# Kernel tuning notes

Hardware: AMD Instinct MI355X
Metric: run time of the kernel (lower is better)

Reference implementation:

```python
import jax, jax.numpy as jnp
import numpy as np

D_MODEL = 1024
NUM_HEADS = 16
HEAD_DIM = D_MODEL // NUM_HEADS  # 64
SCALE = HEAD_DIM ** -0.5
BIAS_LEN = 128  # min(max_seq_len=512, 128)
ROPE_BASE = 10000.0
LN_EPS = 1e-5


def setup_inputs() -> dict:
    key = jax.random.key(0)
    ks = jax.random.split(key, 8)
    B, Lq, Lkv = 8, 512, 512
    return {
        "decoder_hidden": jax.random.normal(ks[0], (B, Lq, D_MODEL), jnp.float32),
        "encoder_output": jax.random.normal(ks[1], (B, Lkv, D_MODEL), jnp.float32),
        "Wqkv": jax.random.normal(ks[2], (3 * D_MODEL, D_MODEL), jnp.float32) * 0.02,
        "Wout": jax.random.normal(ks[3], (D_MODEL, D_MODEL), jnp.float32) * 0.02,
        "b_out": jnp.zeros((D_MODEL,), jnp.float32),
        "Wgate": jax.random.normal(ks[4], (D_MODEL, D_MODEL), jnp.float32) * 0.02,
        "b_gate": jnp.zeros((D_MODEL,), jnp.float32),
        "gamma": jnp.ones((D_MODEL,), jnp.float32),
        "beta": jnp.zeros((D_MODEL,), jnp.float32),
    }


def _layernorm(x, gamma, beta):
    mu = jnp.mean(x, axis=-1, keepdims=True)
    var = jnp.mean(jnp.square(x - mu), axis=-1, keepdims=True)
    return (x - mu) * jax.lax.rsqrt(var + LN_EPS) * gamma + beta


def _rope(x, cos, sin):
    # x: [B, H, L, HEAD_DIM]; cos/sin: [L, HEAD_DIM//2]
    half = HEAD_DIM // 2
    c = cos[None, None, :, :]
    s = sin[None, None, :, :]
    x_even, x_odd = x[..., :half], x[..., half:]
    return jnp.concatenate([x_even * c - x_odd * s, x_even * s + x_odd * c], axis=-1)


def _temporal_bias(L_q, L_kv):
    pos = jnp.arange(BIAS_LEN, dtype=jnp.float32)
    dist = jnp.abs(pos[None, :] - pos[:, None])  # [128,128]
    bias = jnp.exp(-dist * 0.1) - dist * 0.05
    if L_q <= BIAS_LEN and L_kv <= BIAS_LEN:
        return bias[:L_q, :L_kv]
    # bilinear interpolation (align_corners=False / half-pixel) fallback
    return jax.image.resize(bias, (L_q, L_kv), method="bilinear")


def reference(decoder_hidden, encoder_output, Wqkv, Wout, b_out, Wgate, b_gate, gamma, beta):
    B, L_q, _ = decoder_hidden.shape
    L_kv = encoder_output.shape[1]
    residual = decoder_hidden

    q_in = _layernorm(decoder_hidden, gamma, beta)
    kv_in = _layernorm(encoder_output, gamma, beta)

    q = q_in @ Wqkv[:D_MODEL].T
    k = kv_in @ Wqkv[D_MODEL:2 * D_MODEL].T
    v = kv_in @ Wqkv[2 * D_MODEL:].T

    q = q.reshape(B, L_q, NUM_HEADS, HEAD_DIM).transpose(0, 2, 1, 3)
    k = k.reshape(B, L_kv, NUM_HEADS, HEAD_DIM).transpose(0, 2, 1, 3)
    v = v.reshape(B, L_kv, NUM_HEADS, HEAD_DIM).transpose(0, 2, 1, 3)

    # rotary embedding over max(L_q, L_kv) positions
    L = max(L_q, L_kv)
    inv_freq = 1.0 / ROPE_BASE ** (jnp.arange(0, HEAD_DIM, 2, dtype=jnp.float32) / HEAD_DIM)
    freqs = jnp.arange(L, dtype=jnp.float32)[:, None] * inv_freq[None, :]  # [L, HEAD_DIM//2]
    cos, sin = jnp.cos(freqs), jnp.sin(freqs)
    q = _rope(q, cos[:L_q], sin[:L_q])
    k = _rope(k, cos[:L_kv], sin[:L_kv])

    scores = jnp.einsum("bhqd,bhkd->bhqk", q, k) * SCALE
    scores = scores + _temporal_bias(L_q, L_kv)[None, None, :, :]

    attn = jax.nn.softmax(scores, axis=-1)
    attended = jnp.einsum("bhqk,bhkd->bhqd", attn, v)
    attended = attended.transpose(0, 2, 1, 3).reshape(B, L_q, D_MODEL)
    attended = attended @ Wout.T + b_out

    gate = jax.nn.sigmoid(attended @ Wgate.T + b_gate)
    output = gate * attended + (1.0 - gate) * residual
    return output
```

## Files before the change

### kernel.cpp

```cpp
#include <hip/hip_runtime.h>
#include <hip/hip_bf16.h>

#define D_MODEL 1024
#define NHEADS 16
#define HDIM 64
#define BATCH 8
#define SEQ 512
#define NROWS 4096
#define SCALE 0.125f
#define LN_EPS 1e-5f

typedef __attribute__((ext_vector_type(8))) short bf16x8;
typedef __attribute__((ext_vector_type(4))) float f32x4;
typedef __attribute__((ext_vector_type(8))) unsigned short u16x8;

static __device__ __forceinline__ float bf2f(unsigned short u) {
    return __uint_as_float(((unsigned int)u) << 16);
}
static __device__ __forceinline__ unsigned short f2bf(float f) {
    unsigned int x = __float_as_uint(f);
    unsigned int r = (x + 0x7fffu + ((x >> 16) & 1u)) >> 16;
    return (unsigned short)r;
}

#define GLOAD16(gp, lp)                                                        \
    __builtin_amdgcn_global_load_lds(                                          \
        (const __attribute__((address_space(1))) void*)(gp),                   \
        (__attribute__((address_space(3))) void*)(lp), 16, 0, 0)

static __device__ __forceinline__ float bias128(int a, int b) {
    float d = fabsf((float)(a - b));
    return expf(-d * 0.1f) - d * 0.05f;
}

__global__ void prep_kernel(const float* __restrict__ dec, const float* __restrict__ enc,
                            const float* __restrict__ gamma, const float* __restrict__ beta,
                            const float* __restrict__ Wqkv,
                            const float* __restrict__ Wout, const float* __restrict__ Wgate,
                            unsigned short* __restrict__ q_ln, unsigned short* __restrict__ kv_ln,
                            float* __restrict__ bias, unsigned short* __restrict__ Wqkv_bf,
                            unsigned short* __restrict__ Wout_bf, unsigned short* __restrict__ Wgate_bf) {
    int blk = blockIdx.x;
    int t = threadIdx.x;
    if (blk >= 12288) {
        int idx = (blk - 12288) * 256 + t;
        const float* src; unsigned short* dst; int off;
        if (idx < 262144) { src = Wout; dst = Wout_bf; off = idx; }
        else              { src = Wgate; dst = Wgate_bf; off = idx - 262144; }
        float4 v = ((const float4*)src)[off];
        ushort4 u;
        u.x = f2bf(v.x); u.y = f2bf(v.y); u.z = f2bf(v.z); u.w = f2bf(v.w);
        ((ushort4*)dst)[off] = u;
        return;
    }
    if (blk >= 9216) {
        int idx = (blk - 9216) * 256 + t;
        float4 v = ((const float4*)Wqkv)[idx];
        ushort4 u;
        u.x = f2bf(v.x); u.y = f2bf(v.y); u.z = f2bf(v.z); u.w = f2bf(v.w);
        ((ushort4*)Wqkv_bf)[idx] = u;
        return;
    }
    if (blk >= 8192) {
        int idx = (blk - 8192) * 256 + t;
        int qi = idx >> 9, kj = idx & 511;
        float fq = (qi + 0.5f) * 0.25f - 0.5f;
        float fk = (kj + 0.5f) * 0.25f - 0.5f;
        int iq = (int)floorf(fq); float tq = fq - (float)iq;
        int ik = (int)floorf(fk); float tk = fk - (float)ik;
        int iq0 = min(max(iq, 0), 127), iq1 = min(max(iq + 1, 0), 127);
        int ik0 = min(max(ik, 0), 127), ik1 = min(max(ik + 1, 0), 127);
        float v = (1.f - tq) * ((1.f - tk) * bias128(iq0, ik0) + tk * bias128(iq0, ik1))
                +        tq  * ((1.f - tk) * bias128(iq1, ik0) + tk * bias128(iq1, ik1));
        bias[idx] = v;
        return;
    }
    int row = blk;
    const float* src = (row < NROWS) ? dec + (size_t)row * D_MODEL
                                     : enc + (size_t)(row - NROWS) * D_MODEL;
    unsigned short* dst = (row < NROWS) ? q_ln + (size_t)row * D_MODEL
                                        : kv_ln + (size_t)(row - NROWS) * D_MODEL;
    float4 x = ((const float4*)src)[t];
    float s  = x.x + x.y + x.z + x.w;
    float ss = x.x * x.x + x.y * x.y + x.z * x.z + x.w * x.w;
    #pragma unroll
    for (int off = 32; off > 0; off >>= 1) {
        s  += __shfl_down(s, off);
        ss += __shfl_down(ss, off);
    }
    __shared__ float red_s[4], red_ss[4];
    int wid = t >> 6, lane = t & 63;
    if (lane == 0) { red_s[wid] = s; red_ss[wid] = ss; }
    __syncthreads();
    if (t == 0) {
        float S = red_s[0] + red_s[1] + red_s[2] + red_s[3];
        float SS = red_ss[0] + red_ss[1] + red_ss[2] + red_ss[3];
        red_s[0] = S; red_ss[0] = SS;
    }
    __syncthreads();
    float mu  = red_s[0] * (1.0f / 1024.0f);
    float var = red_ss[0] * (1.0f / 1024.0f) - mu * mu;
    float rstd = rsqrtf(var + LN_EPS);
    float4 g = ((const float4*)gamma)[t];
    float4 bb = ((const float4*)beta)[t];
    ushort4 u;
    u.x = f2bf((x.x - mu) * rstd * g.x + bb.x);
    u.y = f2bf((x.y - mu) * rstd * g.y + bb.y);
    u.z = f2bf((x.z - mu) * rstd * g.z + bb.z);
    u.w = f2bf((x.w - mu) * rstd * g.w + bb.w);
    ((ushort4*)dst)[t] = u;
}

__global__ void convert_og(const float* __restrict__ Wout, const float* __restrict__ Wgate,
                           unsigned short* __restrict__ Wout_bf, unsigned short* __restrict__ Wgate_bf) {
    int idx = blockIdx.x * 256 + threadIdx.x;
    const float* src; unsigned short* dst; int off;
    if (idx < 262144) { src = (const float*)Wout; dst = Wout_bf; off = idx; }
    else              { src = (const float*)Wgate; dst = Wgate_bf; off = idx - 262144; }
    float4 v = ((const float4*)src)[off];
    ushort4 u;
    u.x = f2bf(v.x); u.y = f2bf(v.y); u.z = f2bf(v.z); u.w = f2bf(v.w);
    ((ushort4*)dst)[off] = u;
}

#define CSTR 136

struct alignas(16) Smem64B {
    unsigned short A[64 * 128];
    unsigned short B[128 * 128];
};

union alignas(16) Smem64Q {
    struct { unsigned short A[64 * 128]; unsigned short B[128 * 128]; } ab;
    unsigned short C[64 * CSTR];
};

#define MF(a, b, d) __builtin_amdgcn_mfma_f32_16x16x32_bf16((a), (b), (d), 0, 0, 0)

#define GEMM_KH2B(kh)                                                          \
    {                                                                          \
        int pofs = (((kh) * 4 + quad) ^ c) * 8;                                \
        const unsigned short* Arow_ = &As2[(wr * 32 + c) * 128 + pofs];        \
        const unsigned short* Brow_ = &Bs2[(wc * 64 + c) * 128 + pofs];        \
        bf16x8 f0 = *(const bf16x8*)(Arow_);                                   \
        bf16x8 f1 = *(const bf16x8*)(Arow_ + 2048);                            \
        bf16x8 g0 = *(const bf16x8*)(Brow_);                                   \
        bf16x8 g1 = *(const bf16x8*)(Brow_ + 2048);                            \
        bf16x8 g2 = *(const bf16x8*)(Brow_ + 4096);                            \
        bf16x8 g3 = *(const bf16x8*)(Brow_ + 6144);                            \
        c00 = MF(f0, g0, c00); c01 = MF(f0, g1, c01); c02 = MF(f0, g2, c02); c03 = MF(f0, g3, c03); \
        c10 = MF(f1, g0, c10); c11 = MF(f1, g1, c11); c12 = MF(f1, g2, c12); c13 = MF(f1, g3, c13); \
    }

#define GEMM_BODY_64B(Aptr, Bptr)                                              \
    int wave = tid >> 6, lane = tid & 63, quad = lane >> 4, c = lane & 15;     \
    int wr = wave >> 1, wc = wave & 1;                                         \
    int l4 = lane >> 4, l15 = lane & 15;                                       \
    const unsigned short* Abase = (Aptr) + (size_t)(rt * 64) * 1024;           \
    const unsigned short* Bbase = (Bptr) + (size_t)(ct * 128) * 1024;          \
    int aoff0 = (wave * 16 +  0 + l4) * 1024 + ((l15 ^ ( 0 + l4)) * 8);        \
    int aoff1 = (wave * 16 +  4 + l4) * 1024 + ((l15 ^ ( 4 + l4)) * 8);        \
    int aoff2 = (wave * 16 +  8 + l4) * 1024 + ((l15 ^ ( 8 + l4)) * 8);        \
    int aoff3 = (wave * 16 + 12 + l4) * 1024 + ((l15 ^ (12 + l4)) * 8);        \
    int boff0 = (wave * 32 +  0 + l4) * 1024 + ((l15 ^ (( 0 + l4) & 15)) * 8); \
    int boff1 = (wave * 32 +  4 + l4) * 1024 + ((l15 ^ (( 4 + l4) & 15)) * 8); \
    int boff2 = (wave * 32 +  8 + l4) * 1024 + ((l15 ^ (( 8 + l4) & 15)) * 8); \
    int boff3 = (wave * 32 + 12 + l4) * 1024 + ((l15 ^ ((12 + l4) & 15)) * 8); \
    int boff4 = (wave * 32 + 16 + l4) * 1024 + ((l15 ^ ((16 + l4) & 15)) * 8); \
    int boff5 = (wave * 32 + 20 + l4) * 1024 + ((l15 ^ ((20 + l4) & 15)) * 8); \
    int boff6 = (wave * 32 + 24 + l4) * 1024 + ((l15 ^ ((24 + l4) & 15)) * 8); \
    int boff7 = (wave * 32 + 28 + l4) * 1024 + ((l15 ^ ((28 + l4) & 15)) * 8); \
    unsigned short* AsW = As2 + wave * 2048;                                   \
    unsigned short* BsW = Bs2 + wave * 4096;                                   \
    f32x4 c00 = (f32x4)0.f, c01 = (f32x4)0.f, c02 = (f32x4)0.f, c03 = (f32x4)0.f; \
    f32x4 c10 = (f32x4)0.f, c11 = (f32x4)0.f, c12 = (f32x4)0.f, c13 = (f32x4)0.f; \
    for (int kt = 0; kt < 8; ++kt) {                                           \
        int k0 = kt * 128;                                                     \
        __syncthreads();                                                       \
        GLOAD16(Abase + aoff0 + k0, AsW);                                      \
        GLOAD16(Abase + aoff1 + k0, AsW + 512);                                \
        GLOAD16(Abase + aoff2 + k0, AsW + 1024);                               \
        GLOAD16(Abase + aoff3 + k0, AsW + 1536);                               \
        GLOAD16(Bbase + boff0 + k0, BsW);                                      \
        GLOAD16(Bbase + boff1 + k0, BsW + 512);                                \
        GLOAD16(Bbase + boff2 + k0, BsW + 1024);                               \
        GLOAD16(Bbase + boff3 + k0, BsW + 1536);                               \
        GLOAD16(Bbase + boff4 + k0, BsW + 2048);                               \
        GLOAD16(Bbase + boff5 + k0, BsW + 2560);                               \
        GLOAD16(Bbase + boff6 + k0, BsW + 3072);                               \
        GLOAD16(Bbase + boff7 + k0, BsW + 3584);                               \
        __syncthreads();                                                       \
        GEMM_KH2B(0)                                                           \
        GEMM_KH2B(1)                                                           \
        GEMM_KH2B(2)                                                           \
        GEMM_KH2B(3)                                                           \
    }

#define QROPE_REG(i, reg, A0, A1, A2, A3)                                      \
    {                                                                          \
        int mloc = wr * 32 + (i) * 16 + quad * 4 + (reg);                      \
        int crow = mloc * CSTR + wc * 64;                                      \
        float fl = (float)((rt * 64 + mloc) & 511);                            \
        float aa0 = fl * inv0, aa1 = fl * inv1;                                \
        float c0 = cosf(aa0), s0 = sinf(aa0);                                  \
        float c1 = cosf(aa1), s1 = sinf(aa1);                                  \
        float e0 = A0[(reg)], o0 = A2[(reg)];                                  \
        float e1 = A1[(reg)], o1 = A3[(reg)];                                  \
        smemq.C[crow + c]      = f2bf(e0 * c0 - o0 * s0);                      \
        smemq.C[crow + 32 + c] = f2bf(e0 * s0 + o0 * c0);                      \
        smemq.C[crow + 16 + c] = f2bf(e1 * c1 - o1 * s1);                      \
        smemq.C[crow + 48 + c] = f2bf(e1 * s1 + o1 * c1);                      \
    }
#define QROPE_ROW(i, A0, A1, A2, A3)                                           \
    QROPE_REG(i, 0, A0, A1, A2, A3) QROPE_REG(i, 1, A0, A1, A2, A3)            \
    QROPE_REG(i, 2, A0, A1, A2, A3) QROPE_REG(i, 3, A0, A1, A2, A3)

#define QVSEC_REG(i, reg, A0, A1, A2, A3)                                      \
    {                                                                          \
        int crow = (wr * 32 + (i) * 16 + quad * 4 + (reg)) * CSTR + wc * 64;   \
        smemq.C[crow + c]      = f2bf(A0[(reg)]);                              \
        smemq.C[crow + 16 + c] = f2bf(A1[(reg)]);                              \
        smemq.C[crow + 32 + c] = f2bf(A2[(reg)]);                              \
        smemq.C[crow + 48 + c] = f2bf(A3[(reg)]);                              \
    }
#define QVSEC_ROW(i, A0, A1, A2, A3)                                           \
    QVSEC_REG(i, 0, A0, A1, A2, A3) QVSEC_REG(i, 1, A0, A1, A2, A3)            \
    QVSEC_REG(i, 2, A0, A1, A2, A3) QVSEC_REG(i, 3, A0, A1, A2, A3)

__global__ __launch_bounds__(256, 1)
void qkv_gemm_mfma(const unsigned short* __restrict__ q_ln,
                   const unsigned short* __restrict__ kv_ln,
                   const unsigned short* __restrict__ Wb,
                   unsigned short* __restrict__ qo,
                   unsigned short* __restrict__ ko,
                   unsigned short* __restrict__ vo) {
    int bid = blockIdx.x;
    int st = bid >> 5, in = bid & 31;
    int stc = st % 3, str = st / 3;
    int ct = stc * 8 + (in & 7);
    int rt = str * 4 + (in >> 3);
    int n0 = ct * 128;
    int section = n0 >> 10;
    const unsigned short* A = (section == 0) ? q_ln : kv_ln;

    __shared__ Smem64Q smemq;
    unsigned short* As2 = smemq.ab.A;
    unsigned short* Bs2 = smemq.ab.B;
    int tid = threadIdx.x;

    GEMM_BODY_64B(A, Wb)

    __syncthreads();
    if (section == 2) {
        QVSEC_ROW(0, c00, c01, c02, c03)
        QVSEC_ROW(1, c10, c11, c12, c13)
    } else {
        float inv0 = expf(-0.2878231366f * (float)c);
        float inv1 = expf(-0.2878231366f * (float)(16 + c));
        QROPE_ROW(0, c00, c01, c02, c03)
        QROPE_ROW(1, c10, c11, c12, c13)
    }
    __syncthreads();

    unsigned short* outp = (section == 0) ? qo : (section == 1) ? ko : vo;
    int rr = tid >> 2;
    int ch = (tid >> 1) & 1;
    int sub = tid & 1;
    int mm = rt * 64 + rr;
    int bb = mm >> 9, ll = mm & 511;
    int h = ((n0 & 1023) >> 6) + ch;
    unsigned short* orow = outp + (((size_t)bb * NHEADS + h) * SEQ + ll) * HDIM + sub * 32;
    const unsigned short* csrc = &smemq.C[rr * CSTR + ch * 64 + sub * 32];
    #pragma unroll
    for (int kc = 0; kc < 4; ++kc)
        *(u16x8*)(orow + kc * 8) = *(const u16x8*)(csrc + kc * 8);
}

#define O1_REG(mb, reg, n, Acc)                                                \
    t_bf[(size_t)((mb) + (reg)) * 1024 + (n)] = f2bf(Acc[(reg)] + bo);
#define O1_TILE(i, j, Acc)                                                     \
    {                                                                          \
        int n = ct * 128 + wc * 64 + (j) * 16 + c;                             \
        float bo = b_out[n];                                                   \
        int mb = rt * 64 + wr * 32 + (i) * 16 + quad * 4;                      \
        O1_REG(mb, 0, n, Acc) O1_REG(mb, 1, n, Acc)                            \
        O1_REG(mb, 2, n, Acc) O1_REG(mb, 3, n, Acc)                            \
    }

__global__ __launch_bounds__(256, 1)
void out_gemm1_mfma(const unsigned short* __restrict__ att,
                    const unsigned short* __restrict__ Wob,
                    const float* __restrict__ b_out,
                    unsigned short* __restrict__ t_bf) {
    int ct = blockIdx.x, rt = blockIdx.y;
    __shared__ Smem64B smem2;
    unsigned short* As2 = smem2.A;
    unsigned short* Bs2 = smem2.B;
    int tid = threadIdx.x;

    GEMM_BODY_64B(att, Wob)

    O1_TILE(0, 0, c00) O1_TILE(0, 1, c01) O1_TILE(0, 2, c02) O1_TILE(0, 3, c03)
    O1_TILE(1, 0, c10) O1_TILE(1, 1, c11) O1_TILE(1, 2, c12) O1_TILE(1, 3, c13)
}

#define O2_REG(mb, reg, n, Acc)                                                \
    {                                                                          \
        float gz = Acc[(reg)] + bg;                                            \
        float g = 1.0f / (1.0f + expf(-gz));                                   \
        size_t idx = (size_t)((mb) + (reg)) * 1024 + (n);                      \
        float tv = bf2f(t_bf[idx]);                                            \
        float rv = residual[idx];                                              \
        out[idx] = g * tv + (1.0f - g) * rv;                                   \
    }
#define O2_TILE(i, j, Acc)                                                     \
    {                                                                          \
        int n = ct * 128 + wc * 64 + (j) * 16 + c;                             \
        float bg = b_gate[n];                                                  \
        int mb = rt * 64 + wr * 32 + (i) * 16 + quad * 4;                      \
        O2_REG(mb, 0, n, Acc) O2_REG(mb, 1, n, Acc)                            \
        O2_REG(mb, 2, n, Acc) O2_REG(mb, 3, n, Acc)                            \
    }

__global__ __launch_bounds__(256, 1)
void out_gemm2_mfma(const unsigned short* __restrict__ t_bf,
                    const unsigned short* __restrict__ Wgb,
                    const float* __restrict__ b_gate,
                    const float* __restrict__ residual,
                    float* __restrict__ out) {
    int ct = blockIdx.x, rt = blockIdx.y;
    __shared__ Smem64B smem2;
    unsigned short* As2 = smem2.A;
    unsigned short* Bs2 = smem2.B;
    int tid = threadIdx.x;

    GEMM_BODY_64B(t_bf, Wgb)

    O2_TILE(0, 0, c00) O2_TILE(0, 1, c01) O2_TILE(0, 2, c02) O2_TILE(0, 3, c03)
    O2_TILE(1, 0, c10) O2_TILE(1, 1, c11) O2_TILE(1, 2, c12) O2_TILE(1, 3, c13)
}

#define KSTR 72

__global__ __launch_bounds__(512)
void attn_kernel(const unsigned short* __restrict__ q,
                 const unsigned short* __restrict__ k,
                 const unsigned short* __restrict__ v,
                 const float* __restrict__ bias,
                 unsigned short* __restrict__ attended) {
    int qt = blockIdx.x, h = blockIdx.y, b = blockIdx.z;
    __shared__ unsigned short Ks[64 * KSTR];
    __shared__ unsigned short Vt[64 * KSTR];
    __shared__ unsigned short Ps[128 * KSTR];
    __shared__ float lf[128];

    int tid = threadIdx.x;
    int wave = tid >> 6, lane = tid & 63;
    int quad = lane >> 4, c = lane & 15;
    int wb = wave * 16;
    size_t headbase = (((size_t)b * NHEADS + h) * SEQ) * HDIM;
    int q0 = qt * 128;

    const unsigned short* qrow = q + headbase + (size_t)(q0 + wb + c) * HDIM;
    bf16x8 aq0 = *(const bf16x8*)(qrow + quad * 8);
    bf16x8 aq1 = *(const bf16x8*)(qrow + 32 + quad * 8);

    int sr = tid >> 3, sc0 = (tid & 7) * 8;

    f32x4 oacc[4];
    #pragma unroll
    for (int t = 0; t < 4; ++t) oacc[t] = (f32x4)0.f;
    float lrow[4];
    #pragma unroll
    for (int r = 0; r < 4; ++r) lrow[r] = 0.f;

    for (int kt = 0; kt < 8; ++kt) {
        int kv0 = kt * 64;
        __syncthreads();
        {
            const unsigned short* krow = k + headbase + (size_t)(kv0 + sr) * HDIM + sc0;
            const unsigned short* vrow = v + headbase + (size_t)(kv0 + sr) * HDIM + sc0;
            u16x8 ka = *(const u16x8*)(krow);
            u16x8 va = *(const u16x8*)(vrow);
            *(u16x8*)&Ks[sr * KSTR + sc0] = ka;
            #pragma unroll
            for (int j = 0; j < 8; ++j) Vt[(sc0 + j) * KSTR + sr] = va[j];
        }
        __syncthreads();

        f32x4 sacc[4];
        #pragma unroll
        for (int nt = 0; nt < 4; ++nt) {
            const unsigned short* kbase = &Ks[(nt * 16 + c) * KSTR];
            bf16x8 b0 = *(const bf16x8*)(kbase + quad * 8);
            bf16x8 b1 = *(const bf16x8*)(kbase + 32 + quad * 8);
            f32x4 a = (f32x4)0.f;
            a = __builtin_amdgcn_mfma_f32_16x16x32_bf16(aq0, b0, a, 0, 0, 0);
            a = __builtin_amdgcn_mfma_f32_16x16x32_bf16(aq1, b1, a, 0, 0, 0);
            sacc[nt] = a;
        }

        const float* bbase = bias + (size_t)(q0 + wb + quad * 4) * 512 + kv0 + c;
        float tsum[4];
        #pragma unroll
        for (int r = 0; r < 4; ++r) tsum[r] = 0.f;
        #pragma unroll
        for (int nt = 0; nt < 4; ++nt)
            #pragma unroll
            for (int r = 0; r < 4; ++r) {
                float p = __expf(sacc[nt][r] * SCALE + bbase[(size_t)r * 512 + nt * 16]);
                tsum[r] += p;
                Ps[(wb + quad * 4 + r) * KSTR + nt * 16 + c] = f2bf(p);
            }
        #pragma unroll
        for (int r = 0; r < 4; ++r) {
            float t = tsum[r];
            t += __shfl_xor(t, 1);
            t += __shfl_xor(t, 2);
            t += __shfl_xor(t, 4);
            t += __shfl_xor(t, 8);
            lrow[r] += t;
        }

        bf16x8 pb0 = *(const bf16x8*)&Ps[(wb + c) * KSTR + quad * 8];
        bf16x8 pb1 = *(const bf16x8*)&Ps[(wb + c) * KSTR + 32 + quad * 8];
        #pragma unroll
        for (int t = 0; t < 4; ++t) {
            const unsigned short* vbase = &Vt[(t * 16 + c) * KSTR];
            bf16x8 a0 = *(const bf16x8*)(vbase + quad * 8);
            bf16x8 a1 = *(const bf16x8*)(vbase + 32 + quad * 8);
            oacc[t] = __builtin_amdgcn_mfma_f32_16x16x32_bf16(a0, pb0, oacc[t], 0, 0, 0);
            oacc[t] = __builtin_amdgcn_mfma_f32_16x16x32_bf16(a1, pb1, oacc[t], 0, 0, 0);
        }
    }

    if (c == 0) {
        f32x4 lv;
        lv[0] = lrow[0]; lv[1] = lrow[1]; lv[2] = lrow[2]; lv[3] = lrow[3];
        *(f32x4*)&lf[wb + quad * 4] = lv;
    }
    float invl = 1.0f / lf[wb + c];
    unsigned short* drow = attended + ((size_t)b * SEQ + (q0 + wb + c)) * D_MODEL + h * HDIM;
    #pragma unroll
    for (int t = 0; t < 4; ++t) {
        ushort4 o;
        o.x = f2bf(oacc[t][0] * invl);
        o.y = f2bf(oacc[t][1] * invl);
        o.z = f2bf(oacc[t][2] * invl);
        o.w = f2bf(oacc[t][3] * invl);
        *(ushort4*)(drow + t * 16 + quad * 4) = o;
    }
}

extern "C" void kernel_launch(void* const* d_in, const int* in_sizes, int n_in,
                              void* d_out, int out_size, void* d_ws, size_t ws_size,
                              hipStream_t stream) {
    const float* dec    = (const float*)d_in[0];
    const float* enc    = (const float*)d_in[1];
    const float* Wqkv   = (const float*)d_in[2];
    const float* Wout   = (const float*)d_in[3];
    const float* b_out  = (const float*)d_in[4];
    const float* Wgate  = (const float*)d_in[5];
    const float* b_gate = (const float*)d_in[6];
    const float* gamma  = (const float*)d_in[7];
    const float* beta   = (const float*)d_in[8];
    float* out = (float*)d_out;

    char* ws = (char*)d_ws;
    const size_t MB = 1024 * 1024;
    unsigned short* q_ln    = (unsigned short*)(ws + 0 * MB);
    unsigned short* kv_ln   = (unsigned short*)(ws + 8 * MB);
    unsigned short* qb      = (unsigned short*)(ws + 16 * MB);
    unsigned short* kb      = (unsigned short*)(ws + 24 * MB);
    unsigned short* vb      = (unsigned short*)(ws + 32 * MB);
    unsigned short* Wqkv_bf = (unsigned short*)(ws + 40 * MB);
    float*          bias    = (float*)(ws + 46 * MB);
    unsigned short* att     = (unsigned short*)(ws + 0 * MB);
    unsigned short* t_bf    = (unsigned short*)(ws + 24 * MB);

    bool hoist = (ws_size >= 51 * MB);
    unsigned short* Wout_bf  = (unsigned short*)(ws + (hoist ? 47 * MB : 32 * MB));
    unsigned short* Wgate_bf = (unsigned short*)(ws + (hoist ? 49 * MB : 34 * MB));

    prep_kernel<<<hoist ? 14336 : 12288, 256, 0, stream>>>(
        dec, enc, gamma, beta, Wqkv, Wout, Wgate,
        q_ln, kv_ln, bias, Wqkv_bf, Wout_bf, Wgate_bf);
    qkv_gemm_mfma<<<1536, 256, 0, stream>>>(q_ln, kv_ln, Wqkv_bf, qb, kb, vb);
    attn_kernel<<<dim3(4, 16, 8), 512, 0, stream>>>(qb, kb, vb, bias, att);
    if (!hoist)
        convert_og<<<2048, 256, 0, stream>>>(Wout, Wgate, Wout_bf, Wgate_bf);
    out_gemm1_mfma<<<dim3(8, 64), 256, 0, stream>>>(att, Wout_bf, b_out, t_bf);
    out_gemm2_mfma<<<dim3(8, 64), 256, 0, stream>>>(t_bf, Wgate_bf, b_gate, dec, out);
}
```

Measured before the change: 215.6 us.

## Store V pre-transposed from QKV GEMM and use direct-to-LDS swizzled loads in attention

The QKV GEMM epilogue for the V section now transposes the tile through shared memory and writes V in [b,h,d,l] layout. The attention kernel can then load K and V tiles with GLOAD16 (apparently direct global-to-LDS) into XOR-swizzled unpadded buffers, instead of scattering V element by element into a transposed LDS tile. This removes the per-element transpose stores and the register staging in the attention inner loop. The cost is an extra barrier and a transposed store pattern in the GEMM epilogue.

```diff
diff --git a/kernel.cpp b/kernel.cpp
--- a/kernel.cpp
+++ b/kernel.cpp
@@ -133,6 +133,7 @@
 union alignas(16) Smem64Q {
     struct { unsigned short A[64 * 128]; unsigned short B[128 * 128]; } ab;
     unsigned short C[64 * CSTR];
+    unsigned short Ct[128 * 72];
 };
 
 #define MF(a, b, d) __builtin_amdgcn_mfma_f32_16x16x32_bf16((a), (b), (d), 0, 0, 0)
@@ -215,17 +216,11 @@
     QROPE_REG(i, 0, A0, A1, A2, A3) QROPE_REG(i, 1, A0, A1, A2, A3)            \
     QROPE_REG(i, 2, A0, A1, A2, A3) QROPE_REG(i, 3, A0, A1, A2, A3)
 
-#define QVSEC_REG(i, reg, A0, A1, A2, A3)                                      \
-    {                                                                          \
-        int crow = (wr * 32 + (i) * 16 + quad * 4 + (reg)) * CSTR + wc * 64;   \
-        smemq.C[crow + c]      = f2bf(A0[(reg)]);                              \
-        smemq.C[crow + 16 + c] = f2bf(A1[(reg)]);                              \
-        smemq.C[crow + 32 + c] = f2bf(A2[(reg)]);                              \
-        smemq.C[crow + 48 + c] = f2bf(A3[(reg)]);                              \
-    }
-#define QVSEC_ROW(i, A0, A1, A2, A3)                                           \
-    QVSEC_REG(i, 0, A0, A1, A2, A3) QVSEC_REG(i, 1, A0, A1, A2, A3)            \
-    QVSEC_REG(i, 2, A0, A1, A2, A3) QVSEC_REG(i, 3, A0, A1, A2, A3)
+#define QVSECT_REG(i, j, reg, Acc)                                             \
+    smemq.Ct[(wc * 64 + (j) * 16 + c) * 72 + (wr * 32 + (i) * 16 + quad * 4 + (reg))] = f2bf(Acc[(reg)]);
+#define QVSECT_TILE(i, j, Acc)                                                 \
+    QVSECT_REG(i, j, 0, Acc) QVSECT_REG(i, j, 1, Acc)                          \
+    QVSECT_REG(i, j, 2, Acc) QVSECT_REG(i, j, 3, Acc)
 
 __global__ __launch_bounds__(256, 1)
 void qkv_gemm_mfma(const unsigned short* __restrict__ q_ln,
@@ -252,17 +247,29 @@
 
     __syncthreads();
     if (section == 2) {
-        QVSEC_ROW(0, c00, c01, c02, c03)
-        QVSEC_ROW(1, c10, c11, c12, c13)
-    } else {
-        float inv0 = expf(-0.2878231366f * (float)c);
-        float inv1 = expf(-0.2878231366f * (float)(16 + c));
-        QROPE_ROW(0, c00, c01, c02, c03)
-        QROPE_ROW(1, c10, c11, c12, c13)
-    }
+        QVSECT_TILE(0, 0, c00) QVSECT_TILE(0, 1, c01) QVSECT_TILE(0, 2, c02) QVSECT_TILE(0, 3, c03)
+        QVSECT_TILE(1, 0, c10) QVSECT_TILE(1, 1, c11) QVSECT_TILE(1, 2, c12) QVSECT_TILE(1, 3, c13)
+        __syncthreads();
+        int dr = tid >> 1, hh = tid & 1;
+        int h = ((n0 & 1023) >> 6) + (dr >> 6);
+        int d = dr & 63;
+        int mmb = rt * 64;
+        int bb = mmb >> 9, ll0 = mmb & 511;
+        unsigned short* orow = vo + (((size_t)bb * NHEADS + h) * HDIM + d) * SEQ + ll0 + hh * 32;
+        const unsigned short* csrc = &smemq.Ct[dr * 72 + hh * 32];
+        #pragma unroll
+        for (int kc = 0; kc < 4; ++kc)
+            *(u16x8*)(orow + kc * 8) = *(const u16x8*)(csrc + kc * 8);
+        return;
+    }
+
+    float inv0 = expf(-0.2878231366f * (float)c);
+    float inv1 = expf(-0.2878231366f * (float)(16 + c));
+    QROPE_ROW(0, c00, c01, c02, c03)
+    QROPE_ROW(1, c10, c11, c12, c13)
     __syncthreads();
 
-    unsigned short* outp = (section == 0) ? qo : (section == 1) ? ko : vo;
+    unsigned short* outp = (section == 0) ? qo : ko;
     int rr = tid >> 2;
     int ch = (tid >> 1) & 1;
     int sub = tid & 1;
@@ -345,12 +352,12 @@
 __global__ __launch_bounds__(512)
 void attn_kernel(const unsigned short* __restrict__ q,
                  const unsigned short* __restrict__ k,
-                 const unsigned short* __restrict__ v,
+                 const unsigned short* __restrict__ vt,
                  const float* __restrict__ bias,
                  unsigned short* __restrict__ attended) {
     int qt = blockIdx.x, h = blockIdx.y, b = blockIdx.z;
-    __shared__ unsigned short Ks[64 * KSTR];
-    __shared__ unsigned short Vt[64 * KSTR];
+    __shared__ unsigned short Ks[64 * 64];
+    __shared__ unsigned short Vs[64 * 64];
     __shared__ unsigned short Ps[128 * KSTR];
     __shared__ float lf[128];
 
@@ -365,7 +372,15 @@
     bf16x8 aq0 = *(const bf16x8*)(qrow + quad * 8);
     bf16x8 aq1 = *(const bf16x8*)(qrow + 32 + quad * 8);
 
-    int sr = tid >> 3, sc0 = (tid & 7) * 8;
+    int srow = wave * 8 + (lane >> 3);
+    int schunk = (lane & 7) ^ (srow & 7);
+    unsigned short* KsW = Ks + wave * 512;
+    unsigned short* VsW = Vs + wave * 512;
+    const unsigned short* kgb = k + headbase + (size_t)srow * HDIM + schunk * 8;
+    const unsigned short* vgb = vt + headbase + (size_t)srow * SEQ + schunk * 8;
+    int x7 = c & 7;
+    int p0 = (quad ^ x7) * 8;
+    int p1 = ((4 + quad) ^ x7) * 8;
 
     f32x4 oacc[4];
     #pragma unroll
@@ -377,23 +392,16 @@
     for (int kt = 0; kt < 8; ++kt) {
         int kv0 = kt * 64;
         __syncthreads();
-        {
-            const unsigned short* krow = k + headbase + (size_t)(kv0 + sr) * HDIM + sc0;
-            const unsigned short* vrow = v + headbase + (size_t)(kv0 + sr) * HDIM + sc0;
-            u16x8 ka = *(const u16x8*)(krow);
-            u16x8 va = *(const u16x8*)(vrow);
-            *(u16x8*)&Ks[sr * KSTR + sc0] = ka;
-            #pragma unroll
-            for (int j = 0; j < 8; ++j) Vt[(sc0 + j) * KSTR + sr] = va[j];
-        }
+        GLOAD16(kgb + (size_t)kv0 * HDIM, KsW);
+        GLOAD16(vgb + kv0, VsW);
         __syncthreads();
 
         f32x4 sacc[4];
         #pragma unroll
         for (int nt = 0; nt < 4; ++nt) {
-            const unsigned short* kbase = &Ks[(nt * 16 + c) * KSTR];
-            bf16x8 b0 = *(const bf16x8*)(kbase + quad * 8);
-            bf16x8 b1 = *(const bf16x8*)(kbase + 32 + quad * 8);
+            const unsigned short* kbase = &Ks[(nt * 16 + c) * 64];
+            bf16x8 b0 = *(const bf16x8*)(kbase + p0);
+            bf16x8 b1 = *(const bf16x8*)(kbase + p1);
             f32x4 a = (f32x4)0.f;
             a = __builtin_amdgcn_mfma_f32_16x16x32_bf16(aq0, b0, a, 0, 0, 0);
             a = __builtin_amdgcn_mfma_f32_16x16x32_bf16(aq1, b1, a, 0, 0, 0);
@@ -426,9 +434,9 @@
         bf16x8 pb1 = *(const bf16x8*)&Ps[(wb + c) * KSTR + 32 + quad * 8];
         #pragma unroll
         for (int t = 0; t < 4; ++t) {
-            const unsigned short* vbase = &Vt[(t * 16 + c) * KSTR];
-            bf16x8 a0 = *(const bf16x8*)(vbase + quad * 8);
-            bf16x8 a1 = *(const bf16x8*)(vbase + 32 + quad * 8);
+            const unsigned short* vbase = &Vs[(t * 16 + c) * 64];
+            bf16x8 a0 = *(const bf16x8*)(vbase + p0);
+            bf16x8 a1 = *(const bf16x8*)(vbase + p1);
             oacc[t] = __builtin_amdgcn_mfma_f32_16x16x32_bf16(a0, pb0, oacc[t], 0, 0, 0);
             oacc[t] = __builtin_amdgcn_mfma_f32_16x16x32_bf16(a1, pb1, oacc[t], 0, 0, 0);
         }
```

Result: no change. 212.9 us (-1.3%).
